# Performance work log

Hardware: AMD Instinct MI355X
Metric: run time of the kernel (lower is better)

The kernel has to match this reference:

```python
import jax, jax.numpy as jnp
import numpy as np

HID, H, KV, S, B = 2048, 32, 8, 2048, 2
D = HID // H           # head_dim = 64
G = H // KV            # query heads per kv head = 4


def setup_inputs() -> dict:
    key = jax.random.key(0)
    ks = jax.random.split(key, 10)
    sc = 0.02
    kv_dim = HID * KV // H  # 512
    return {
        "x": jax.random.normal(ks[0], (B, S, HID), jnp.float32),
        "attention_mask": jnp.zeros((B, S), jnp.float32),
        "Wq": jax.random.normal(ks[1], (HID, HID), jnp.float32) * sc,
        "bq": jnp.zeros((HID,), jnp.float32),
        "Wk": jax.random.normal(ks[2], (kv_dim, HID), jnp.float32) * sc,
        "bk": jnp.zeros((kv_dim,), jnp.float32),
        "Wv": jax.random.normal(ks[3], (kv_dim, HID), jnp.float32) * sc,
        "bv": jnp.zeros((kv_dim,), jnp.float32),
        "Wo": jax.random.normal(ks[4], (HID, HID), jnp.float32) * sc,
        "bo": jnp.zeros((HID,), jnp.float32),
    }


def reference(x, attention_mask, Wq, bq, Wk, bk, Wv, bv, Wo, bo):
    Bx, Sx, _ = x.shape
    # projections (torch Linear: x @ W.T + b)
    q = x @ Wq.T + bq                                  # [B,S,HID]
    k = x @ Wk.T + bk                                  # [B,S,KV*D]
    v = x @ Wv.T + bv
    # split heads: [B,S,H,D] -> [B,H,S,D]; then group q: [B,KV,G,S,D]
    q = q.reshape(Bx, Sx, H, D).transpose(0, 2, 1, 3).reshape(Bx, KV, G, Sx, D)
    k = k.reshape(Bx, Sx, KV, D).transpose(0, 2, 1, 3)  # [B,KV,S,D]
    v = v.reshape(Bx, Sx, KV, D).transpose(0, 2, 1, 3)
    scale = 1.0 / jnp.sqrt(jnp.float32(D))
    scores = jnp.einsum('bkgsd,bktd->bkgst', q, k) * scale  # [B,KV,G,S,S]
    scores = scores + attention_mask[:, None, None, None, :]
    attn = jax.nn.softmax(scores, axis=-1)
    out = jnp.einsum('bkgst,bktd->bkgsd', attn, v)          # [B,KV,G,S,D]
    out = out.reshape(Bx, H, Sx, D).transpose(0, 2, 1, 3).reshape(Bx, Sx, HID)
    return out @ Wo.T + bo
```

## Files before the change

kernel.cpp:

```cpp
#include <hip/hip_runtime.h>
#include <hip/hip_bf16.h>
#include <stdint.h>

typedef __hip_bfloat16 bf16;
typedef __attribute__((ext_vector_type(8))) short bf16x8;
typedef __attribute__((ext_vector_type(4))) float f32x4;
typedef __attribute__((ext_vector_type(16))) float f32x16;
typedef __attribute__((ext_vector_type(4))) int i32x4;
typedef __attribute__((ext_vector_type(2))) int i32x2;

#define B_   2
#define S_   2048
#define HID_ 2048
#define H_   32
#define KV_  8
#define D_   64
#define NT_  (S_ / 64)
#define LOG2E 1.4426950408889634f

__device__ __forceinline__ void gload_lds16(const void* g, void* l) {
  __builtin_amdgcn_global_load_lds(
      (const __attribute__((address_space(1))) uint32_t*)g,
      (__attribute__((address_space(3))) uint32_t*)l, 16, 0, 0);
}
__device__ __forceinline__ float fexp2(float x) { return __builtin_amdgcn_exp2f(x); }

__device__ __forceinline__ uint32_t cvtpk_bf16(float lo, float hi) {
  uint32_t r;
  asm("v_cvt_pk_bf16_f32 %0, %1, %2" : "=v"(r) : "v"(lo), "v"(hi));
  return r;
}
__device__ __forceinline__ void plane32_swap(uint32_t& a, uint32_t& b) {
  i32x2 r = __builtin_amdgcn_permlane32_swap((int)a, (int)b, false, false);
  a = (uint32_t)r[0]; b = (uint32_t)r[1];
}

struct CvtJob { const float* s; bf16* d; int n4; };
__global__ __launch_bounds__(256) void cvt_multi(
    CvtJob j0, CvtJob j1, CvtJob j2, CvtJob j3, CvtJob j4) {
  CvtJob j;
  switch (blockIdx.y) {
    case 0: j = j0; break;
    case 1: j = j1; break;
    case 2: j = j2; break;
    case 3: j = j3; break;
    default: j = j4; break;
  }
  int i = blockIdx.x * blockDim.x + threadIdx.x;
  const int stride = gridDim.x * blockDim.x;
  for (; i < j.n4; i += stride) {
    float4 v = ((const float4*)j.s)[i];
    bf16 t[4];
    t[0] = __float2bfloat16(v.x);
    t[1] = __float2bfloat16(v.y);
    t[2] = __float2bfloat16(v.z);
    t[3] = __float2bfloat16(v.w);
    *reinterpret_cast<uint64_t*>(j.d + 4 * (size_t)i) = *reinterpret_cast<uint64_t*>(t);
  }
}

__global__ __launch_bounds__(256) void mask_prep(
    const float* __restrict__ m, float* __restrict__ o, int n) {
  int i = blockIdx.x * blockDim.x + threadIdx.x;
  if (i < n) o[i] = m[i] * LOG2E;
}

__global__ __launch_bounds__(256, 2) void gemm_qkv(
    const bf16* __restrict__ A,
    const bf16* __restrict__ Wqp, const bf16* __restrict__ Wkp, const bf16* __restrict__ Wvp,
    const float* __restrict__ bqp, const float* __restrict__ bkp, const float* __restrict__ bvp,
    bf16* __restrict__ Cq, bf16* __restrict__ Ck, bf16* __restrict__ Cv) {
  const int lid0 = blockIdx.y * gridDim.x + blockIdx.x;
  const int q8 = (int)(gridDim.x * gridDim.y) >> 3;
  const int lid = (lid0 & 7) * q8 + (lid0 >> 3);
  const int bm = lid & 31;
  const int bn_all = lid >> 5;

  const bf16* W; const float* bias; int bn;
  if (bn_all < 16)      { W = Wqp; bias = bqp; bn = bn_all; }
  else if (bn_all < 20) { W = Wkp; bias = bkp; bn = bn_all - 16; }
  else                  { W = Wvp; bias = bvp; bn = bn_all - 20; }
  const float oscale = (bn_all < 16) ? (0.125f * LOG2E) : 1.0f;

  __shared__ __align__(16) bf16 As[128 * 64];
  __shared__ __align__(16) bf16 Bs[128 * 64];
  const int tid = threadIdx.x;
  const int lane = tid & 63, wid = tid >> 6;
  const int wr = wid >> 1, wc = wid & 1;
  const int K = HID_;

  f32x4 acc[4][4] = {};

  for (int k0 = 0; k0 < K; k0 += 64) {
    __syncthreads();
#pragma unroll
    for (int c = 0; c < 4; ++c) {
      const int r = c * 32 + wid * 8 + (lane >> 3);
      const int gcolb = ((lane & 7) * 16) ^ ((r & 7) << 4);
      gload_lds16(A + (size_t)(bm * 128 + r) * K + k0 + (gcolb >> 1),
                  &As[(c * 32 + wid * 8) * 64]);
      gload_lds16(W + (size_t)(bn * 128 + r) * K + k0 + (gcolb >> 1),
                  &Bs[(c * 32 + wid * 8) * 64]);
    }
    __syncthreads();
#pragma unroll
    for (int ks = 0; ks < 2; ++ks) {
      bf16x8 af[4], bfr[4];
#pragma unroll
      for (int i = 0; i < 4; ++i) {
        const int ra = wr * 64 + i * 16 + (lane & 15);
        const int ka = (ks * 64 + ((lane >> 4) << 4)) ^ ((ra & 7) << 4);
        af[i] = *(const bf16x8*)((const char*)As + ra * 128 + ka);
        const int rb = wc * 64 + i * 16 + (lane & 15);
        const int kb = (ks * 64 + ((lane >> 4) << 4)) ^ ((rb & 7) << 4);
        bfr[i] = *(const bf16x8*)((const char*)Bs + rb * 128 + kb);
      }
      __builtin_amdgcn_s_setprio(1);
#pragma unroll
      for (int i = 0; i < 4; ++i)
#pragma unroll
        for (int j = 0; j < 4; ++j)
          acc[i][j] = __builtin_amdgcn_mfma_f32_16x16x32_bf16(af[i], bfr[j], acc[i][j], 0, 0, 0);
      __builtin_amdgcn_s_setprio(0);
    }
  }

  if (bn_all < 20) {
    const int Hn = (bn_all < 16) ? H_ : KV_;
    bf16* C = (bn_all < 16) ? Cq : Ck;
#pragma unroll
    for (int j = 0; j < 4; ++j) {
      const int n = bn * 128 + wc * 64 + j * 16 + (lane & 15);
      const float bv = bias[n];
#pragma unroll
      for (int i = 0; i < 4; ++i) {
        const int mb = bm * 128 + wr * 64 + i * 16 + ((lane >> 4) << 2);
#pragma unroll
        for (int e = 0; e < 4; ++e) {
          const int m = mb + e;
          const float v = (acc[i][j][e] + bv) * oscale;
          const int b = m >> 11, s = m & (S_ - 1);
          const int h = n >> 6, d = n & 63;
          C[(((size_t)b * Hn + h) * S_ + s) * 64 + d] = __float2bfloat16(v);
        }
      }
    }
  } else {
#pragma unroll
    for (int j = 0; j < 4; ++j) {
      const int n = bn * 128 + wc * 64 + j * 16 + (lane & 15);
      const int kvh = n >> 6, d = n & 63;
      const float bv = bias[n];
#pragma unroll
      for (int i = 0; i < 4; ++i) {
        const int m0 = bm * 128 + wr * 64 + i * 16 + ((lane >> 4) << 2);
        const int b = m0 >> 11, s0 = m0 & (S_ - 1);
        bf16 t4[4];
#pragma unroll
        for (int e = 0; e < 4; ++e) t4[e] = __float2bfloat16(acc[i][j][e] + bv);
        *reinterpret_cast<uint64_t*>(
            Cv + (((size_t)b * KV_ + kvh) * D_ + d) * S_ + s0) =
            *reinterpret_cast<uint64_t*>(t4);
      }
    }
  }
}

__global__ __launch_bounds__(256, 2) void gemm_out(
    const bf16* __restrict__ A, const bf16* __restrict__ W,
    const float* __restrict__ bias, float* __restrict__ C) {
  const int lid0 = blockIdx.y * gridDim.x + blockIdx.x;
  const int q8 = (int)(gridDim.x * gridDim.y) >> 3;
  const int lid = (lid0 & 7) * q8 + (lid0 >> 3);
  const int bm = lid & 31;
  const int bn = lid >> 5;

  __shared__ __align__(16) bf16 As[128 * 64];
  __shared__ __align__(16) bf16 Bs[128 * 64];
  const int tid = threadIdx.x;
  const int lane = tid & 63, wid = tid >> 6;
  const int wr = wid >> 1, wc = wid & 1;
  const int K = HID_, N = HID_;

  f32x4 acc[4][4] = {};

  for (int k0 = 0; k0 < K; k0 += 64) {
    __syncthreads();
#pragma unroll
    for (int c = 0; c < 4; ++c) {
      const int r = c * 32 + wid * 8 + (lane >> 3);
      const int gcolb = ((lane & 7) * 16) ^ ((r & 7) << 4);
      gload_lds16(A + (size_t)(bm * 128 + r) * K + k0 + (gcolb >> 1),
                  &As[(c * 32 + wid * 8) * 64]);
      gload_lds16(W + (size_t)(bn * 128 + r) * K + k0 + (gcolb >> 1),
                  &Bs[(c * 32 + wid * 8) * 64]);
    }
    __syncthreads();
#pragma unroll
    for (int ks = 0; ks < 2; ++ks) {
      bf16x8 af[4], bfr[4];
#pragma unroll
      for (int i = 0; i < 4; ++i) {
        const int ra = wr * 64 + i * 16 + (lane & 15);
        const int ka = (ks * 64 + ((lane >> 4) << 4)) ^ ((ra & 7) << 4);
        af[i] = *(const bf16x8*)((const char*)As + ra * 128 + ka);
        const int rb = wc * 64 + i * 16 + (lane & 15);
        const int kb = (ks * 64 + ((lane >> 4) << 4)) ^ ((rb & 7) << 4);
        bfr[i] = *(const bf16x8*)((const char*)Bs + rb * 128 + kb);
      }
      __builtin_amdgcn_s_setprio(1);
#pragma unroll
      for (int i = 0; i < 4; ++i)
#pragma unroll
        for (int j = 0; j < 4; ++j)
          acc[i][j] = __builtin_amdgcn_mfma_f32_16x16x32_bf16(af[i], bfr[j], acc[i][j], 0, 0, 0);
      __builtin_amdgcn_s_setprio(0);
    }
  }

#pragma unroll
  for (int j = 0; j < 4; ++j) {
    const int n = bn * 128 + wc * 64 + j * 16 + (lane & 15);
    const float bv = bias[n];
#pragma unroll
    for (int i = 0; i < 4; ++i) {
      const int mb = bm * 128 + wr * 64 + i * 16 + ((lane >> 4) << 2);
#pragma unroll
      for (int e = 0; e < 4; ++e) {
        C[(size_t)(mb + e) * N + n] = acc[i][j][e] + bv;
      }
    }
  }
}

__global__ __launch_bounds__(256, 2) void attn_fwd(
    const bf16* __restrict__ qb, const bf16* __restrict__ kb,
    const bf16* __restrict__ vtb, const float* __restrict__ maskL,
    bf16* __restrict__ ob) {
  const int lid0 = blockIdx.y * gridDim.x + blockIdx.x;
  const int q8 = (int)(gridDim.x * gridDim.y) >> 3;
  const int lid = (lid0 & 7) * q8 + (lid0 >> 3);
  const int qtile = lid & 7;
  const int headid = lid >> 3;
  const int b = headid >> 5, h = headid & (H_ - 1);
  const int kv = h >> 2;
  const int tid = threadIdx.x, lane = tid & 63, wid = tid >> 6;
  const int l31 = lane & 31, hi = lane >> 5;

  __shared__ __align__(16) bf16 Ks[2][64 * 64];
  __shared__ __align__(16) bf16 VTs[2][64 * 64];
  __shared__ float lsm[4][64];

  const bf16* qh = qb + ((size_t)(b * H_ + h) * S_) * D_;
  const bf16* kh = kb + ((size_t)(b * KV_ + kv) * S_) * D_;
  const bf16* vth = vtb + (size_t)(b * KV_ + kv) * D_ * S_;
  const float* mrow = maskL + (size_t)b * S_;

  const int qrowbase = qtile * 256 + wid * 64;
  bf16x8 qf[2][4];
#pragma unroll
  for (int qs = 0; qs < 2; ++qs)
#pragma unroll
    for (int ks = 0; ks < 4; ++ks)
      qf[qs][ks] = *(const bf16x8*)(qh + (size_t)(qrowbase + qs * 32 + l31) * D_ + ks * 16 + hi * 8);

  float lp0 = 0.f, lp1 = 0.f;
  f32x16 o0[2] = {}, o1[2] = {};

#pragma unroll
  for (int c = 0; c < 2; ++c) {
    const int r = c * 32 + wid * 8 + (lane >> 3);
    const int gcolb = ((lane & 7) * 16) ^ ((r & 7) << 4);
    gload_lds16(kh + (size_t)r * D_ + (gcolb >> 1), &Ks[0][(c * 32 + wid * 8) * 64]);
    gload_lds16(vth + (size_t)r * S_ + (gcolb >> 1), &VTs[0][(c * 32 + wid * 8) * 64]);
  }
  __syncthreads();

  for (int t = 0; t < NT_; ++t) {
    const int cur = t & 1, nxt = cur ^ 1;

    if (t < NT_ - 1) {
#pragma unroll
      for (int c = 0; c < 2; ++c) {
        const int r = c * 32 + wid * 8 + (lane >> 3);
        const int gcolb = ((lane & 7) * 16) ^ ((r & 7) << 4);
        gload_lds16(kh + ((size_t)(t + 1) * 64 + r) * D_ + (gcolb >> 1),
                    &Ks[nxt][(c * 32 + wid * 8) * 64]);
        gload_lds16(vth + (size_t)r * S_ + (t + 1) * 64 + (gcolb >> 1),
                    &VTs[nxt][(c * 32 + wid * 8) * 64]);
      }
    }

    f32x16 s0[2], s1[2];
#pragma unroll
    for (int kbv = 0; kbv < 2; ++kbv) {
#pragma unroll
      for (int rq = 0; rq < 4; ++rq) {
        const f32x4 m4 = *(const f32x4*)(mrow + t * 64 + kbv * 32 + rq * 8 + 4 * hi);
#pragma unroll
        for (int e = 0; e < 4; ++e) {
          s0[kbv][rq * 4 + e] = m4[e];
          s1[kbv][rq * 4 + e] = m4[e];
        }
      }
    }
#pragma unroll
    for (int kbv = 0; kbv < 2; ++kbv) {
      __builtin_amdgcn_s_setprio(1);
#pragma unroll
      for (int ks = 0; ks < 4; ++ks) {
        const int rk = kbv * 32 + l31;
        const int kbyte = (ks * 32 + hi * 16) ^ ((rk & 7) << 4);
        bf16x8 kf = *(const bf16x8*)((const char*)&Ks[cur][0] + rk * 128 + kbyte);
        s0[kbv] = __builtin_amdgcn_mfma_f32_32x32x16_bf16(kf, qf[0][ks], s0[kbv], 0, 0, 0);
        s1[kbv] = __builtin_amdgcn_mfma_f32_32x32x16_bf16(kf, qf[1][ks], s1[kbv], 0, 0, 0);
      }
      __builtin_amdgcn_s_setprio(0);
    }

    {
      float2 a0 = make_float2(0.f, 0.f), a1 = make_float2(0.f, 0.f);
#pragma unroll
      for (int kbv = 0; kbv < 2; ++kbv)
#pragma unroll
        for (int r8 = 0; r8 < 8; ++r8) {
          const float p00 = fexp2(s0[kbv][2 * r8]);
          const float p01 = fexp2(s0[kbv][2 * r8 + 1]);
          const float p10 = fexp2(s1[kbv][2 * r8]);
          const float p11 = fexp2(s1[kbv][2 * r8 + 1]);
          s0[kbv][2 * r8] = p00; s0[kbv][2 * r8 + 1] = p01;
          s1[kbv][2 * r8] = p10; s1[kbv][2 * r8 + 1] = p11;
          a0.x += p00; a0.y += p01;
          a1.x += p10; a1.y += p11;
        }
      lp0 += a0.x + a0.y;
      lp1 += a1.x + a1.y;
    }

    bf16x8 pa0[2][2], pa1[2][2];
#pragma unroll
    for (int kbv = 0; kbv < 2; ++kbv) {
      {
        uint32_t a0 = cvtpk_bf16(s0[kbv][0], s0[kbv][1]);
        uint32_t b0 = cvtpk_bf16(s0[kbv][4], s0[kbv][5]);
        plane32_swap(a0, b0);
        uint32_t a1 = cvtpk_bf16(s0[kbv][2], s0[kbv][3]);
        uint32_t b1 = cvtpk_bf16(s0[kbv][6], s0[kbv][7]);
        plane32_swap(a1, b1);
        i32x4 t0; t0[0] = (int)a0; t0[1] = (int)a1; t0[2] = (int)b0; t0[3] = (int)b1;
        pa0[kbv][0] = __builtin_bit_cast(bf16x8, t0);
        uint32_t a2 = cvtpk_bf16(s0[kbv][8], s0[kbv][9]);
        uint32_t b2 = cvtpk_bf16(s0[kbv][12], s0[kbv][13]);
        plane32_swap(a2, b2);
        uint32_t a3 = cvtpk_bf16(s0[kbv][10], s0[kbv][11]);
        uint32_t b3 = cvtpk_bf16(s0[kbv][14], s0[kbv][15]);
        plane32_swap(a3, b3);
        i32x4 t1; t1[0] = (int)a2; t1[1] = (int)a3; t1[2] = (int)b2; t1[3] = (int)b3;
        pa0[kbv][1] = __builtin_bit_cast(bf16x8, t1);
      }
      {
        uint32_t a0 = cvtpk_bf16(s1[kbv][0], s1[kbv][1]);
        uint32_t b0 = cvtpk_bf16(s1[kbv][4], s1[kbv][5]);
        plane32_swap(a0, b0);
        uint32_t a1 = cvtpk_bf16(s1[kbv][2], s1[kbv][3]);
        uint32_t b1 = cvtpk_bf16(s1[kbv][6], s1[kbv][7]);
        plane32_swap(a1, b1);
        i32x4 t0; t0[0] = (int)a0; t0[1] = (int)a1; t0[2] = (int)b0; t0[3] = (int)b1;
        pa1[kbv][0] = __builtin_bit_cast(bf16x8, t0);
        uint32_t a2 = cvtpk_bf16(s1[kbv][8], s1[kbv][9]);
        uint32_t b2 = cvtpk_bf16(s1[kbv][12], s1[kbv][13]);
        plane32_swap(a2, b2);
        uint32_t a3 = cvtpk_bf16(s1[kbv][10], s1[kbv][11]);
        uint32_t b3 = cvtpk_bf16(s1[kbv][14], s1[kbv][15]);
        plane32_swap(a3, b3);
        i32x4 t1; t1[0] = (int)a2; t1[1] = (int)a3; t1[2] = (int)b2; t1[3] = (int)b3;
        pa1[kbv][1] = __builtin_bit_cast(bf16x8, t1);
      }
    }

#pragma unroll
    for (int db = 0; db < 2; ++db) {
      __builtin_amdgcn_s_setprio(1);
#pragma unroll
      for (int kbv = 0; kbv < 2; ++kbv)
#pragma unroll
        for (int ks2 = 0; ks2 < 2; ++ks2) {
          const int rd = db * 32 + l31;
          const int vbyte = (kbv * 64 + ks2 * 32 + hi * 16) ^ ((rd & 7) << 4);
          bf16x8 vf = *(const bf16x8*)((const char*)&VTs[cur][0] + rd * 128 + vbyte);
          o0[db] = __builtin_amdgcn_mfma_f32_32x32x16_bf16(pa0[kbv][ks2], vf, o0[db], 0, 0, 0);
          o1[db] = __builtin_amdgcn_mfma_f32_32x32x16_bf16(pa1[kbv][ks2], vf, o1[db], 0, 0, 0);
        }
      __builtin_amdgcn_s_setprio(0);
    }

    __syncthreads();
  }

  {
    uint32_t la = __float_as_uint(lp0), lb = la;
    plane32_swap(la, lb);
    lsm[wid][l31] = __uint_as_float(la) + __uint_as_float(lb);
    uint32_t lc = __float_as_uint(lp1), ld = lc;
    plane32_swap(lc, ld);
    lsm[wid][32 + l31] = __uint_as_float(lc) + __uint_as_float(ld);
  }
  __syncthreads();
#pragma unroll
  for (int qs = 0; qs < 2; ++qs) {
#pragma unroll
    for (int rq = 0; rq < 4; ++rq) {
      const f32x4 l4 = *(const f32x4*)&lsm[wid][qs * 32 + rq * 8 + 4 * hi];
#pragma unroll
      for (int e2 = 0; e2 < 4; ++e2) {
        const float inv = 1.0f / l4[e2];
        const int q_out = e2 + 8 * rq + 4 * hi;
        const int srow = qrowbase + qs * 32 + q_out;
#pragma unroll
        for (int db = 0; db < 2; ++db) {
          const float val = (qs == 0 ? o0[db][rq * 4 + e2] : o1[db][rq * 4 + e2]) * inv;
          ob[((size_t)b * S_ + srow) * HID_ + h * 64 + db * 32 + l31] = __float2bfloat16(val);
        }
      }
    }
  }
}

extern "C" void kernel_launch(void* const* d_in, const int* in_sizes, int n_in,
                              void* d_out, int out_size, void* d_ws, size_t ws_size,
                              hipStream_t stream) {
  (void)in_sizes; (void)n_in; (void)out_size; (void)ws_size;
  const float* x  = (const float*)d_in[0];
  const float* am = (const float*)d_in[1];
  const float* Wq = (const float*)d_in[2];
  const float* bq = (const float*)d_in[3];
  const float* Wk = (const float*)d_in[4];
  const float* bk = (const float*)d_in[5];
  const float* Wv = (const float*)d_in[6];
  const float* bv = (const float*)d_in[7];
  const float* Wo = (const float*)d_in[8];
  const float* bo = (const float*)d_in[9];
  float* out = (float*)d_out;

  const size_t XE  = (size_t)B_ * S_ * HID_;
  const size_t WQE = (size_t)HID_ * HID_;
  const size_t WKE = (size_t)(KV_ * D_) * HID_;
  const size_t QE  = (size_t)B_ * H_ * S_ * D_;
  const size_t KE  = (size_t)B_ * KV_ * S_ * D_;

  bf16* xb  = (bf16*)d_ws;
  bf16* wqb = xb + XE;
  bf16* wkb = wqb + WQE;
  bf16* wvb = wkb + WKE;
  bf16* wob = wvb + WKE;
  bf16* qbuf = wob + WQE;
  bf16* kbuf = qbuf + QE;
  bf16* vtbuf = kbuf + KE;
  bf16* abuf = vtbuf + KE;
  float* maskL = (float*)(abuf + XE);

  dim3 blk(256);
  CvtJob jx  = { x,  xb,  (int)(XE / 4) };
  CvtJob jwq = { Wq, wqb, (int)(WQE / 4) };
  CvtJob jwk = { Wk, wkb, (int)(WKE / 4) };
  CvtJob jwv = { Wv, wvb, (int)(WKE / 4) };
  CvtJob jwo = { Wo, wob, (int)(WQE / 4) };
  cvt_multi<<<dim3(512, 5), blk, 0, stream>>>(jx, jwq, jwk, jwv, jwo);
  mask_prep<<<(B_ * S_ + 255) / 256, blk, 0, stream>>>(am, maskL, B_ * S_);

  const int M = B_ * S_;
  gemm_qkv<<<dim3(M / 128, 24), blk, 0, stream>>>(xb, wqb, wkb, wvb, bq, bk, bv,
                                                  qbuf, kbuf, vtbuf);
  attn_fwd<<<dim3(S_ / 256, B_ * H_), blk, 0, stream>>>(qbuf, kbuf, vtbuf, maskL, abuf);
  gemm_out<<<dim3(M / 128, HID_ / 128), blk, 0, stream>>>(abuf, wob, bo, out);
}
```

Measured before the change: 192.2 us.

## Interleave QK MFMA with exp/pack and compute row sums via ones-MFMA

Restructures the attention inner loop so the score MFMAs for later sub-tiles are issued between the exp2 and bf16 packing of earlier sub-tiles, letting matrix and vector work overlap. Row sums of P are now computed by an extra MFMA against a vector of ones instead of VALU adds followed by a shared-memory reduction, which removes the lsm buffer and the final barrier. The row sums now come from bf16-rounded P rather than fp32 values, and the extra accumulators raise register pressure. The QKV GEMM launch bound is also raised to three blocks per SM.

```diff
diff --git a/kernel.cpp b/kernel.cpp
--- a/kernel.cpp
+++ b/kernel.cpp
@@ -65,7 +65,7 @@
   if (i < n) o[i] = m[i] * LOG2E;
 }
 
-__global__ __launch_bounds__(256, 2) void gemm_qkv(
+__global__ __launch_bounds__(256, 3) void gemm_qkv(
     const bf16* __restrict__ A,
     const bf16* __restrict__ Wqp, const bf16* __restrict__ Wkp, const bf16* __restrict__ Wvp,
     const float* __restrict__ bqp, const float* __restrict__ bkp, const float* __restrict__ bvp,
@@ -249,7 +249,6 @@
 
   __shared__ __align__(16) bf16 Ks[2][64 * 64];
   __shared__ __align__(16) bf16 VTs[2][64 * 64];
-  __shared__ float lsm[4][64];
 
   const bf16* qh = qb + ((size_t)(b * H_ + h) * S_) * D_;
   const bf16* kh = kb + ((size_t)(b * KV_ + kv) * S_) * D_;
@@ -264,8 +263,12 @@
     for (int ks = 0; ks < 4; ++ks)
       qf[qs][ks] = *(const bf16x8*)(qh + (size_t)(qrowbase + qs * 32 + l31) * D_ + ks * 16 + hi * 8);
 
-  float lp0 = 0.f, lp1 = 0.f;
+  bf16x8 ones;
+#pragma unroll
+  for (int i = 0; i < 8; ++i) ones[i] = (short)0x3F80;
+
   f32x16 o0[2] = {}, o1[2] = {};
+  f32x16 lacc0 = {}, lacc1 = {};
 
 #pragma unroll
   for (int c = 0; c < 2; ++c) {
@@ -304,124 +307,155 @@
         }
       }
     }
+
+    bf16x8 kf0[4], kf1[4];
+#pragma unroll
+    for (int ks = 0; ks < 4; ++ks) {
+      const int rk = l31;
+      const int kbyte = (ks * 32 + hi * 16) ^ ((rk & 7) << 4);
+      kf0[ks] = *(const bf16x8*)((const char*)&Ks[cur][0] + rk * 128 + kbyte);
+    }
+    __builtin_amdgcn_s_setprio(1);
+#pragma unroll
+    for (int ks = 0; ks < 4; ++ks)
+      s0[0] = __builtin_amdgcn_mfma_f32_32x32x16_bf16(kf0[ks], qf[0][ks], s0[0], 0, 0, 0);
+#pragma unroll
+    for (int ks = 0; ks < 4; ++ks)
+      s1[0] = __builtin_amdgcn_mfma_f32_32x32x16_bf16(kf0[ks], qf[1][ks], s1[0], 0, 0, 0);
+    __builtin_amdgcn_s_setprio(0);
+#pragma unroll
+    for (int ks = 0; ks < 4; ++ks) {
+      const int rk = 32 + l31;
+      const int kbyte = (ks * 32 + hi * 16) ^ ((rk & 7) << 4);
+      kf1[ks] = *(const bf16x8*)((const char*)&Ks[cur][0] + rk * 128 + kbyte);
+    }
+    __builtin_amdgcn_s_setprio(1);
+#pragma unroll
+    for (int ks = 0; ks < 4; ++ks)
+      s0[1] = __builtin_amdgcn_mfma_f32_32x32x16_bf16(kf1[ks], qf[0][ks], s0[1], 0, 0, 0);
+    __builtin_amdgcn_s_setprio(0);
+
+    bf16x8 pa0[2][2], pa1[2][2];
+#pragma unroll
+    for (int r = 0; r < 16; ++r) s0[0][r] = fexp2(s0[0][r]);
+    {
+      uint32_t a0 = cvtpk_bf16(s0[0][0], s0[0][1]);
+      uint32_t b0 = cvtpk_bf16(s0[0][4], s0[0][5]);
+      plane32_swap(a0, b0);
+      uint32_t a1 = cvtpk_bf16(s0[0][2], s0[0][3]);
+      uint32_t b1 = cvtpk_bf16(s0[0][6], s0[0][7]);
+      plane32_swap(a1, b1);
+      i32x4 t0; t0[0] = (int)a0; t0[1] = (int)a1; t0[2] = (int)b0; t0[3] = (int)b1;
+      pa0[0][0] = __builtin_bit_cast(bf16x8, t0);
+      uint32_t a2 = cvtpk_bf16(s0[0][8], s0[0][9]);
+      uint32_t b2 = cvtpk_bf16(s0[0][12], s0[0][13]);
+      plane32_swap(a2, b2);
+      uint32_t a3 = cvtpk_bf16(s0[0][10], s0[0][11]);
+      uint32_t b3 = cvtpk_bf16(s0[0][14], s0[0][15]);
+      plane32_swap(a3, b3);
+      i32x4 t1; t1[0] = (int)a2; t1[1] = (int)a3; t1[2] = (int)b2; t1[3] = (int)b3;
+      pa0[0][1] = __builtin_bit_cast(bf16x8, t1);
+    }
+
+    __builtin_amdgcn_s_setprio(1);
+#pragma unroll
+    for (int ks = 0; ks < 4; ++ks)
+      s1[1] = __builtin_amdgcn_mfma_f32_32x32x16_bf16(kf1[ks], qf[1][ks], s1[1], 0, 0, 0);
+    __builtin_amdgcn_s_setprio(0);
+
+#pragma unroll
+    for (int r = 0; r < 16; ++r) s0[1][r] = fexp2(s0[1][r]);
+    {
+      uint32_t a0 = cvtpk_bf16(s0[1][0], s0[1][1]);
+      uint32_t b0 = cvtpk_bf16(s0[1][4], s0[1][5]);
+      plane32_swap(a0, b0);
+      uint32_t a1 = cvtpk_bf16(s0[1][2], s0[1][3]);
+      uint32_t b1 = cvtpk_bf16(s0[1][6], s0[1][7]);
+      plane32_swap(a1, b1);
+      i32x4 t0; t0[0] = (int)a0; t0[1] = (int)a1; t0[2] = (int)b0; t0[3] = (int)b1;
+      pa0[1][0] = __builtin_bit_cast(bf16x8, t0);
+      uint32_t a2 = cvtpk_bf16(s0[1][8], s0[1][9]);
+      uint32_t b2 = cvtpk_bf16(s0[1][12], s0[1][13]);
+      plane32_swap(a2, b2);
+      uint32_t a3 = cvtpk_bf16(s0[1][10], s0[1][11]);
+      uint32_t b3 = cvtpk_bf16(s0[1][14], s0[1][15]);
+      plane32_swap(a3, b3);
+      i32x4 t1; t1[0] = (int)a2; t1[1] = (int)a3; t1[2] = (int)b2; t1[3] = (int)b3;
+      pa0[1][1] = __builtin_bit_cast(bf16x8, t1);
+    }
+
+    bf16x8 vf[2][4];
+#pragma unroll
+    for (int db = 0; db < 2; ++db)
+#pragma unroll
+      for (int kk = 0; kk < 4; ++kk) {
+        const int kbv = kk >> 1, ks2 = kk & 1;
+        const int rd = db * 32 + l31;
+        const int vbyte = (kbv * 64 + ks2 * 32 + hi * 16) ^ ((rd & 7) << 4);
+        vf[db][kk] = *(const bf16x8*)((const char*)&VTs[cur][0] + rd * 128 + vbyte);
+      }
+
+    __builtin_amdgcn_s_setprio(1);
+#pragma unroll
+    for (int kk = 0; kk < 4; ++kk)
+      lacc0 = __builtin_amdgcn_mfma_f32_32x32x16_bf16(pa0[kk >> 1][kk & 1], ones, lacc0, 0, 0, 0);
+#pragma unroll
+    for (int db = 0; db < 2; ++db)
+#pragma unroll
+      for (int kk = 0; kk < 4; ++kk)
+        o0[db] = __builtin_amdgcn_mfma_f32_32x32x16_bf16(pa0[kk >> 1][kk & 1], vf[db][kk], o0[db], 0, 0, 0);
+    __builtin_amdgcn_s_setprio(0);
+
 #pragma unroll
     for (int kbv = 0; kbv < 2; ++kbv) {
-      __builtin_amdgcn_s_setprio(1);
-#pragma unroll
-      for (int ks = 0; ks < 4; ++ks) {
-        const int rk = kbv * 32 + l31;
-        const int kbyte = (ks * 32 + hi * 16) ^ ((rk & 7) << 4);
-        bf16x8 kf = *(const bf16x8*)((const char*)&Ks[cur][0] + rk * 128 + kbyte);
-        s0[kbv] = __builtin_amdgcn_mfma_f32_32x32x16_bf16(kf, qf[0][ks], s0[kbv], 0, 0, 0);
-        s1[kbv] = __builtin_amdgcn_mfma_f32_32x32x16_bf16(kf, qf[1][ks], s1[kbv], 0, 0, 0);
-      }
-      __builtin_amdgcn_s_setprio(0);
-    }
-
+#pragma unroll
+      for (int r = 0; r < 16; ++r) s1[kbv][r] = fexp2(s1[kbv][r]);
+      uint32_t a0 = cvtpk_bf16(s1[kbv][0], s1[kbv][1]);
+      uint32_t b0 = cvtpk_bf16(s1[kbv][4], s1[kbv][5]);
+      plane32_swap(a0, b0);
+      uint32_t a1 = cvtpk_bf16(s1[kbv][2], s1[kbv][3]);
+      uint32_t b1 = cvtpk_bf16(s1[kbv][6], s1[kbv][7]);
+      plane32_swap(a1, b1);
+      i32x4 t0; t0[0] = (int)a0; t0[1] = (int)a1; t0[2] = (int)b0; t0[3] = (int)b1;
+      pa1[kbv][0] = __builtin_bit_cast(bf16x8, t0);
+      uint32_t a2 = cvtpk_bf16(s1[kbv][8], s1[kbv][9]);
+      uint32_t b2 = cvtpk_bf16(s1[kbv][12], s1[kbv][13]);
+      plane32_swap(a2, b2);
+      uint32_t a3 = cvtpk_bf16(s1[kbv][10], s1[kbv][11]);
+      uint32_t b3 = cvtpk_bf16(s1[kbv][14], s1[kbv][15]);
+      plane32_swap(a3, b3);
+      i32x4 t1; t1[0] = (int)a2; t1[1] = (int)a3; t1[2] = (int)b2; t1[3] = (int)b3;
+      pa1[kbv][1] = __builtin_bit_cast(bf16x8, t1);
+    }
+
+    __builtin_amdgcn_s_setprio(1);
+#pragma unroll
+    for (int kk = 0; kk < 4; ++kk)
+      lacc1 = __builtin_amdgcn_mfma_f32_32x32x16_bf16(pa1[kk >> 1][kk & 1], ones, lacc1, 0, 0, 0);
+#pragma unroll
+    for (int db = 0; db < 2; ++db)
+#pragma unroll
+      for (int kk = 0; kk < 4; ++kk)
+        o1[db] = __builtin_amdgcn_mfma_f32_32x32x16_bf16(pa1[kk >> 1][kk & 1], vf[db][kk], o1[db], 0, 0, 0);
+    __builtin_amdgcn_s_setprio(0);
+
+    __syncthreads();
+  }
+
+#pragma unroll
+  for (int r = 0; r < 16; ++r) {
+    const int q_out = (r & 3) + 8 * (r >> 2) + 4 * hi;
     {
-      float2 a0 = make_float2(0.f, 0.f), a1 = make_float2(0.f, 0.f);
-#pragma unroll
-      for (int kbv = 0; kbv < 2; ++kbv)
-#pragma unroll
-        for (int r8 = 0; r8 < 8; ++r8) {
-          const float p00 = fexp2(s0[kbv][2 * r8]);
-          const float p01 = fexp2(s0[kbv][2 * r8 + 1]);
-          const float p10 = fexp2(s1[kbv][2 * r8]);
-          const float p11 = fexp2(s1[kbv][2 * r8 + 1]);
-          s0[kbv][2 * r8] = p00; s0[kbv][2 * r8 + 1] = p01;
-          s1[kbv][2 * r8] = p10; s1[kbv][2 * r8 + 1] = p11;
-          a0.x += p00; a0.y += p01;
-          a1.x += p10; a1.y += p11;
-        }
-      lp0 += a0.x + a0.y;
-      lp1 += a1.x + a1.y;
-    }
-
-    bf16x8 pa0[2][2], pa1[2][2];
-#pragma unroll
-    for (int kbv = 0; kbv < 2; ++kbv) {
-      {
-        uint32_t a0 = cvtpk_bf16(s0[kbv][0], s0[kbv][1]);
-        uint32_t b0 = cvtpk_bf16(s0[kbv][4], s0[kbv][5]);
-        plane32_swap(a0, b0);
-        uint32_t a1 = cvtpk_bf16(s0[kbv][2], s0[kbv][3]);
-        uint32_t b1 = cvtpk_bf16(s0[kbv][6], s0[kbv][7]);
-        plane32_swap(a1, b1);
-        i32x4 t0; t0[0] = (int)a0; t0[1] = (int)a1; t0[2] = (int)b0; t0[3] = (int)b1;
-        pa0[kbv][0] = __builtin_bit_cast(bf16x8, t0);
-        uint32_t a2 = cvtpk_bf16(s0[kbv][8], s0[kbv][9]);
-        uint32_t b2 = cvtpk_bf16(s0[kbv][12], s0[kbv][13]);
-        plane32_swap(a2, b2);
-        uint32_t a3 = cvtpk_bf16(s0[kbv][10], s0[kbv][11]);
-        uint32_t b3 = cvtpk_bf16(s0[kbv][14], s0[kbv][15]);
-        plane32_swap(a3, b3);
-        i32x4 t1; t1[0] = (int)a2; t1[1] = (int)a3; t1[2] = (int)b2; t1[3] = (int)b3;
-        pa0[kbv][1] = __builtin_bit_cast(bf16x8, t1);
-      }
-      {
-        uint32_t a0 = cvtpk_bf16(s1[kbv][0], s1[kbv][1]);
-        uint32_t b0 = cvtpk_bf16(s1[kbv][4], s1[kbv][5]);
-        plane32_swap(a0, b0);
-        uint32_t a1 = cvtpk_bf16(s1[kbv][2], s1[kbv][3]);
-        uint32_t b1 = cvtpk_bf16(s1[kbv][6], s1[kbv][7]);
-        plane32_swap(a1, b1);
-        i32x4 t0; t0[0] = (int)a0; t0[1] = (int)a1; t0[2] = (int)b0; t0[3] = (int)b1;
-        pa1[kbv][0] = __builtin_bit_cast(bf16x8, t0);
-        uint32_t a2 = cvtpk_bf16(s1[kbv][8], s1[kbv][9]);
-        uint32_t b2 = cvtpk_bf16(s1[kbv][12], s1[kbv][13]);
-        plane32_swap(a2, b2);
-        uint32_t a3 = cvtpk_bf16(s1[kbv][10], s1[kbv][11]);
-        uint32_t b3 = cvtpk_bf16(s1[kbv][14], s1[kbv][15]);
-        plane32_swap(a3, b3);
-        i32x4 t1; t1[0] = (int)a2; t1[1] = (int)a3; t1[2] = (int)b2; t1[3] = (int)b3;
-        pa1[kbv][1] = __builtin_bit_cast(bf16x8, t1);
-      }
-    }
-
-#pragma unroll
-    for (int db = 0; db < 2; ++db) {
-      __builtin_amdgcn_s_setprio(1);
-#pragma unroll
-      for (int kbv = 0; kbv < 2; ++kbv)
-#pragma unroll
-        for (int ks2 = 0; ks2 < 2; ++ks2) {
-          const int rd = db * 32 + l31;
-          const int vbyte = (kbv * 64 + ks2 * 32 + hi * 16) ^ ((rd & 7) << 4);
-          bf16x8 vf = *(const bf16x8*)((const char*)&VTs[cur][0] + rd * 128 + vbyte);
-          o0[db] = __builtin_amdgcn_mfma_f32_32x32x16_bf16(pa0[kbv][ks2], vf, o0[db], 0, 0, 0);
-          o1[db] = __builtin_amdgcn_mfma_f32_32x32x16_bf16(pa1[kbv][ks2], vf, o1[db], 0, 0, 0);
-        }
-      __builtin_amdgcn_s_setprio(0);
-    }
-
-    __syncthreads();
-  }
-
-  {
-    uint32_t la = __float_as_uint(lp0), lb = la;
-    plane32_swap(la, lb);
-    lsm[wid][l31] = __uint_as_float(la) + __uint_as_float(lb);
-    uint32_t lc = __float_as_uint(lp1), ld = lc;
-    plane32_swap(lc, ld);
-    lsm[wid][32 + l31] = __uint_as_float(lc) + __uint_as_float(ld);
-  }
-  __syncthreads();
-#pragma unroll
-  for (int qs = 0; qs < 2; ++qs) {
-#pragma unroll
-    for (int rq = 0; rq < 4; ++rq) {
-      const f32x4 l4 = *(const f32x4*)&lsm[wid][qs * 32 + rq * 8 + 4 * hi];
-#pragma unroll
-      for (int e2 = 0; e2 < 4; ++e2) {
-        const float inv = 1.0f / l4[e2];
-        const int q_out = e2 + 8 * rq + 4 * hi;
-        const int srow = qrowbase + qs * 32 + q_out;
-#pragma unroll
-        for (int db = 0; db < 2; ++db) {
-          const float val = (qs == 0 ? o0[db][rq * 4 + e2] : o1[db][rq * 4 + e2]) * inv;
-          ob[((size_t)b * S_ + srow) * HID_ + h * 64 + db * 32 + l31] = __float2bfloat16(val);
-        }
-      }
+      const float inv = 1.0f / lacc0[r];
+      const int srow = qrowbase + q_out;
+      ob[((size_t)b * S_ + srow) * HID_ + h * 64 + l31] = __float2bfloat16(o0[0][r] * inv);
+      ob[((size_t)b * S_ + srow) * HID_ + h * 64 + 32 + l31] = __float2bfloat16(o0[1][r] * inv);
+    }
+    {
+      const float inv = 1.0f / lacc1[r];
+      const int srow = qrowbase + 32 + q_out;
+      ob[((size_t)b * S_ + srow) * HID_ + h * 64 + l31] = __float2bfloat16(o1[0][r] * inv);
+      ob[((size_t)b * S_ + srow) * HID_ + h * 64 + 32 + l31] = __float2bfloat16(o1[1][r] * inv);
     }
   }
 }
```

New measurement: 191.8 us. About the same (-0.2%).
